# Kernel tuning notes

Hardware: AMD Instinct MI355X
Metric: run time of the kernel (lower is better)

## Reference

```python
import jax, jax.numpy as jnp
import numpy as np

N_A, N_C, N_L = 50000, 10000, 10000
HID = 128


def _gatv2(x_src, x_dst, src, dst, ea, Wl, bl, Wr, br, We, att, bias, H):
    # GATv2Conv (PyG) bipartite, edge_dim=1, concat=False (mean over heads), eval mode (no dropout)
    C = bias.shape[0]
    n_dst = x_dst.shape[0]
    xl = (x_src @ Wl + bl).reshape(-1, H, C)      # [N_src, H, C]
    xr = (x_dst @ Wr + br).reshape(-1, H, C)      # [N_dst, H, C]
    e = jax.nn.leaky_relu(xl[src] + xr[dst] + (ea @ We).reshape(-1, H, C), 0.2)  # [E,H,C]
    logit = jnp.einsum('ehc,hc->eh', e, att)      # [E,H]
    m = jax.ops.segment_max(logit, dst, num_segments=n_dst)
    m = jax.lax.stop_gradient(jnp.where(jnp.isfinite(m), m, 0.0))
    ex = jnp.exp(logit - m[dst])
    denom = jax.ops.segment_sum(ex, dst, num_segments=n_dst)
    alpha = ex / (denom[dst] + 1e-16)             # segment softmax over incoming edges
    out = jax.ops.segment_sum(alpha[:, :, None] * xl[src], dst, num_segments=n_dst)
    return out.mean(axis=1) + bias                # concat=False -> head mean + bias


def setup_inputs() -> dict:
    key = jax.random.key(0)
    ks = iter(jax.random.split(key, 80))
    def rn(shape, s=1.0):
        return jax.random.normal(next(ks), shape, jnp.float32) * s
    inp = {}
    inp['x_asset'] = rn((N_A, 512))
    inp['x_creator'] = rn((N_C, 2))
    inp['x_licensee'] = rn((N_L, 1))
    # edges: (name, E, src_max, dst_max)
    edges = [('cb', 50000, N_A, N_C), ('lt', 100000, N_A, N_L), ('sim', 200000, N_A, N_A),
             ('fw', 100000, N_A, N_A), ('rcb', 50000, N_C, N_A), ('rlt', 100000, N_L, N_A)]
    for name, E, smax, dmax in edges:
        inp[f'{name}_src'] = jax.random.randint(next(ks), (E,), 0, smax, jnp.int32)
        inp[f'{name}_dst'] = jax.random.randint(next(ks), (E,), 0, dmax, jnp.int32)
        inp[f'ea_{name}'] = rn((E, 1))
    w = 0.05  # param scale
    inp['Wp_a'] = rn((512, HID), w); inp['bp_a'] = rn((HID,), w)
    inp['Wp_c'] = rn((2, HID), w);   inp['bp_c'] = rn((HID,), w)
    inp['Wp_l'] = rn((1, HID), w);   inp['bp_l'] = rn((HID,), w)
    # layer 1: heads=2, stacked over the 6 relations
    H1 = 2
    inp['Wl1'] = rn((6, HID, H1 * HID), w); inp['bl1'] = rn((6, H1 * HID), w)
    inp['Wr1'] = rn((6, HID, H1 * HID), w); inp['br1'] = rn((6, H1 * HID), w)
    inp['We1'] = rn((6, 1, H1 * HID), w)
    inp['att1'] = rn((6, H1, HID), w); inp['bias1'] = rn((6, HID), w)
    # layer 2: heads=1
    inp['Wl2'] = rn((6, HID, HID), w); inp['bl2'] = rn((6, HID), w)
    inp['Wr2'] = rn((6, HID, HID), w); inp['br2'] = rn((6, HID), w)
    inp['We2'] = rn((6, 1, HID), w)
    inp['att2'] = rn((6, 1, HID), w); inp['bias2'] = rn((6, HID), w)
    inp['Wc1'] = rn((HID, HID), w); inp['bc1'] = rn((HID,), w)
    inp['Wc2'] = rn((HID, 3), w);   inp['bc2'] = rn((3,), w)
    inp['query_asset_index'] = 123
    return inp


def reference(x_asset, x_creator, x_licensee, Wp_a, bp_a, Wp_c, bp_c, Wp_l, bp_l,
              Wl1, bl1, Wr1, br1, We1, att1, bias1,
              Wl2, bl2, Wr2, br2, We2, att2, bias2,
              Wc1, bc1, Wc2, bc2,
              ea_cb, ea_lt, ea_sim, ea_fw, ea_rcb, ea_rlt,
              cb_src, cb_dst, lt_src, lt_dst, sim_src, sim_dst,
              fw_src, fw_dst, rcb_src, rcb_dst, rlt_src, rlt_dst,
              query_asset_index):
    x = {'Asset': x_asset @ Wp_a + bp_a,
         'Creator': x_creator @ Wp_c + bp_c,
         'Licensee': x_licensee @ Wp_l + bp_l}
    rels = [('Asset', 'Creator', cb_src, cb_dst, ea_cb),
            ('Asset', 'Licensee', lt_src, lt_dst, ea_lt),
            ('Asset', 'Asset', sim_src, sim_dst, ea_sim),
            ('Asset', 'Asset', fw_src, fw_dst, ea_fw),
            ('Creator', 'Asset', rcb_src, rcb_dst, ea_rcb),
            ('Licensee', 'Asset', rlt_src, rlt_dst, ea_rlt)]

    def hetero_layer(x, Wl, bl, Wr, br, We, att, bias, H):
        out = {k: jnp.zeros((v.shape[0], HID), v.dtype) for k, v in x.items()}
        for i, (st, dt, s, d, ea) in enumerate(rels):  # HeteroConv aggr='sum'
            out[dt] = out[dt] + _gatv2(x[st], x[dt], s, d, ea,
                                       Wl[i], bl[i], Wr[i], br[i], We[i], att[i], bias[i], H)
        return out

    x = hetero_layer(x, Wl1, bl1, Wr1, br1, We1, att1, bias1, 2)
    x = {k: jax.nn.relu(v) for k, v in x.items()}  # eval: dropout is identity
    x = hetero_layer(x, Wl2, bl2, Wr2, br2, We2, att2, bias2, 1)
    x = {k: jax.nn.relu(v) for k, v in x.items()}
    a = x['Asset'][query_asset_index]
    return jax.nn.relu(a @ Wc1 + bc1) @ Wc2 + bc2
```

## Files before the change

kernel.cpp:

```cpp
#include <hip/hip_runtime.h>
#include <math.h>

#define FAMAX 512
#define FCMAX 256
#define FLMAX 256
#define N1MAX 4096
#define N2MAX 512

struct Inputs {
  const float *x_asset, *x_creator, *x_licensee;
  const float *Wp_a,*bp_a,*Wp_c,*bp_c,*Wp_l,*bp_l;
  const float *Wl1,*bl1,*Wr1,*br1,*We1,*att1,*bias1;
  const float *Wl2,*bl2,*Wr2,*br2,*We2,*att2,*bias2;
  const float *Wc1,*bc1,*Wc2,*bc2;
};

struct Edges {
  const int *cb_s,*cb_d;  const float* ea_cb;  int Ecb;
  const int *lt_s,*lt_d;  const float* ea_lt;  int Elt;
  const int *sim_s,*sim_d;const float* ea_sim; int Esim;
  const int *fw_s,*fw_d;  const float* ea_fw;  int Efw;
  const int *rcb_s,*rcb_d;const float* ea_rcb; int Ercb;
  const int *rlt_s,*rlt_d;const float* ea_rlt; int Erlt;
};

struct WSP {
  int* cnt;
  int* flagA; int* flagC; int* flagL;
  int* fa; int* fc; int* fl;
  int* l2rel; int* l2src; float* l2ea;
  int* l1rel; int* l1src; int* l1dslot; float* l1ea;
  float* xr1a;
  float* xr1c;
  float* xr1l;
  float* xl1e;
  float* logit1;
  float* x1a;
  float* x1c;
  float* x1l;
  float* xr2q;
  float* xl2e;
  float* logit2;
};

__device__ __forceinline__ float leaky(float x){ return x > 0.f ? x : 0.2f*x; }

__device__ void proj_node(int type, int node, const Inputs& in, float* h0){
  int t = threadIdx.x;
  if (t < 128) {
    float acc;
    if (type == 0) {
      acc = in.bp_a[t];
      const float* xr = in.x_asset + (long long)node*512;
      for (int k=0;k<512;k++) acc = fmaf(xr[k], in.Wp_a[k*128+t], acc);
    } else if (type == 1) {
      acc = in.bp_c[t] + in.x_creator[node*2]*in.Wp_c[t] + in.x_creator[node*2+1]*in.Wp_c[128+t];
    } else {
      acc = in.bp_l[t] + in.x_licensee[node]*in.Wp_l[t];
    }
    h0[t] = acc;
  }
  __syncthreads();
}

__global__ void k1_scan_l2(Edges eg, const int* qptr, WSP w){
  int q = qptr[0];
  if (blockIdx.x==0 && threadIdx.x==0) w.flagA[q] = 1;
  int total = eg.Esim + eg.Efw + eg.Ercb + eg.Erlt;
  for (int i = blockIdx.x*blockDim.x + threadIdx.x; i < total; i += gridDim.x*blockDim.x){
    int j = i, rel; const int *sp,*dp; const float* ep;
    if (j < eg.Esim){ rel=2; sp=eg.sim_s; dp=eg.sim_d; ep=eg.ea_sim; }
    else { j -= eg.Esim;
      if (j < eg.Efw){ rel=3; sp=eg.fw_s; dp=eg.fw_d; ep=eg.ea_fw; }
      else { j -= eg.Efw;
        if (j < eg.Ercb){ rel=4; sp=eg.rcb_s; dp=eg.rcb_d; ep=eg.ea_rcb; }
        else { j -= eg.Ercb; rel=5; sp=eg.rlt_s; dp=eg.rlt_d; ep=eg.ea_rlt; }
      }
    }
    if (dp[j] == q){
      int src = sp[j];
      int k = atomicAdd(&w.cnt[0], 1);
      if (k < N2MAX){ w.l2rel[k]=rel; w.l2src[k]=src; w.l2ea[k]=ep[j]; }
      if (rel <= 3) w.flagA[src] = 1;
      else if (rel == 4) w.flagC[src] = 1;
      else w.flagL[src] = 1;
    }
  }
}

__global__ void k2_compact(WSP w){
  int i = blockIdx.x*blockDim.x + threadIdx.x;
  if (i < 50000){
    if (w.flagA[i] == 1){ int k = atomicAdd(&w.cnt[1],1);
      if (k < FAMAX){ w.flagA[i]=k+2; w.fa[k]=i; } else w.flagA[i]=0; }
  } else if (i < 60000){ int n=i-50000;
    if (w.flagC[n] == 1){ int k = atomicAdd(&w.cnt[2],1);
      if (k < FCMAX){ w.flagC[n]=k+2; w.fc[k]=n; } else w.flagC[n]=0; }
  } else if (i < 70000){ int n=i-60000;
    if (w.flagL[n] == 1){ int k = atomicAdd(&w.cnt[3],1);
      if (k < FLMAX){ w.flagL[n]=k+2; w.fl[k]=n; } else w.flagL[n]=0; }
  }
}

__global__ void k3_scan_l1(Edges eg, WSP w){
  int total = eg.Ecb+eg.Elt+eg.Esim+eg.Efw+eg.Ercb+eg.Erlt;
  for (int i = blockIdx.x*blockDim.x + threadIdx.x; i < total; i += gridDim.x*blockDim.x){
    int j = i, rel; const int *sp,*dp; const float* ep; const int* flag;
    if (j < eg.Ecb){ rel=0; sp=eg.cb_s; dp=eg.cb_d; ep=eg.ea_cb; flag=w.flagC; }
    else { j -= eg.Ecb;
    if (j < eg.Elt){ rel=1; sp=eg.lt_s; dp=eg.lt_d; ep=eg.ea_lt; flag=w.flagL; }
    else { j -= eg.Elt;
    if (j < eg.Esim){ rel=2; sp=eg.sim_s; dp=eg.sim_d; ep=eg.ea_sim; flag=w.flagA; }
    else { j -= eg.Esim;
    if (j < eg.Efw){ rel=3; sp=eg.fw_s; dp=eg.fw_d; ep=eg.ea_fw; flag=w.flagA; }
    else { j -= eg.Efw;
    if (j < eg.Ercb){ rel=4; sp=eg.rcb_s; dp=eg.rcb_d; ep=eg.ea_rcb; flag=w.flagA; }
    else { j -= eg.Ercb; rel=5; sp=eg.rlt_s; dp=eg.rlt_d; ep=eg.ea_rlt; flag=w.flagA; }}}}}
    int f = flag[dp[j]];
    if (f >= 2){
      int k = atomicAdd(&w.cnt[4], 1);
      if (k < N1MAX){ w.l1rel[k]=rel; w.l1src[k]=sp[j]; w.l1dslot[k]=f-2; w.l1ea[k]=ep[j]; }
    }
  }
}

__global__ void k4_xr1(Inputs in, WSP w){
  __shared__ float h0[128];
  int b = blockIdx.x;
  int na = w.cnt[1] < FAMAX ? w.cnt[1] : FAMAX;
  int nc = w.cnt[2] < FCMAX ? w.cnt[2] : FCMAX;
  int nl = w.cnt[3] < FLMAX ? w.cnt[3] : FLMAX;
  int rel; float* dst;
  if (b < FAMAX*4){
    int slot = b>>2, ridx = b&3;
    if (slot >= na) return;
    rel = 2 + ridx;
    proj_node(0, w.fa[slot], in, h0);
    dst = w.xr1a + ((size_t)slot*4 + ridx)*256;
  } else if (b < FAMAX*4 + FCMAX){
    int slot = b - FAMAX*4;
    if (slot >= nc) return;
    rel = 0;
    proj_node(1, w.fc[slot], in, h0);
    dst = w.xr1c + (size_t)slot*256;
  } else {
    int slot = b - FAMAX*4 - FCMAX;
    if (slot >= nl) return;
    rel = 1;
    proj_node(2, w.fl[slot], in, h0);
    dst = w.xr1l + (size_t)slot*256;
  }
  int j = threadIdx.x;
  float acc = in.br1[rel*256 + j];
  const float* W = in.Wr1 + (size_t)rel*128*256;
  for (int c=0;c<128;c++) acc = fmaf(h0[c], W[c*256 + j], acc);
  dst[j] = acc;
}

__global__ void k5_l1edge(Inputs in, WSP w){
  __shared__ float h0[128];
  __shared__ float red[256];
  int i = blockIdx.x;
  int n = w.cnt[4] < N1MAX ? w.cnt[4] : N1MAX;
  if (i >= n) return;
  int rel = w.l1rel[i], src = w.l1src[i], dslot = w.l1dslot[i];
  float ea = w.l1ea[i];
  int stype = (rel <= 3) ? 0 : (rel == 4 ? 1 : 2);
  proj_node(stype, src, in, h0);
  int j = threadIdx.x;
  float acc = in.bl1[rel*256 + j];
  const float* W = in.Wl1 + (size_t)rel*128*256;
  for (int c=0;c<128;c++) acc = fmaf(h0[c], W[c*256 + j], acc);
  w.xl1e[(size_t)i*256 + j] = acc;
  const float* xr;
  if (rel >= 2) xr = w.xr1a + ((size_t)dslot*4 + (rel-2))*256;
  else if (rel == 0) xr = w.xr1c + (size_t)dslot*256;
  else xr = w.xr1l + (size_t)dslot*256;
  float e = leaky(acc + xr[j] + ea*in.We1[rel*256 + j]);
  int h = j >> 7, c = j & 127;
  red[j] = e * in.att1[(rel*2 + h)*128 + c];
  __syncthreads();
  for (int s=64; s>0; s>>=1){ if (c < s) red[j] += red[j+s]; __syncthreads(); }
  if (c == 0) w.logit1[i*2 + h] = red[j];
}

__global__ void k6_agg(Inputs in, WSP w){
  int b = blockIdx.x;
  int na = w.cnt[1] < FAMAX ? w.cnt[1] : FAMAX;
  int nc = w.cnt[2] < FCMAX ? w.cnt[2] : FCMAX;
  int nl = w.cnt[3] < FLMAX ? w.cnt[3] : FLMAX;
  int type, slot;
  if (b < FAMAX){ slot = b; if (slot >= na) return; type = 0; }
  else if (b < FAMAX+FCMAX){ slot = b-FAMAX; if (slot >= nc) return; type = 1; }
  else { slot = b-FAMAX-FCMAX; if (slot >= nl) return; type = 2; }
  int n1 = w.cnt[4] < N1MAX ? w.cnt[4] : N1MAX;
  int j = threadIdx.x;
  float out = 0.f;
  int r0, r1;
  if (type == 0){ r0=2; r1=5; } else if (type == 1){ r0=0; r1=0; } else { r0=1; r1=1; }
  for (int r=r0; r<=r1; r++){
    out += in.bias1[r*128 + j];
    float m0 = -INFINITY, m1 = -INFINITY;
    for (int i=0;i<n1;i++){
      if (w.l1rel[i]==r && w.l1dslot[i]==slot){
        m0 = fmaxf(m0, w.logit1[i*2]);
        m1 = fmaxf(m1, w.logit1[i*2+1]);
      }
    }
    if (m0 == -INFINITY) continue;
    float d0=0.f, d1=0.f, a0=0.f, a1=0.f;
    for (int i=0;i<n1;i++){
      if (w.l1rel[i]==r && w.l1dslot[i]==slot){
        float e0 = expf(w.logit1[i*2]   - m0);
        float e1 = expf(w.logit1[i*2+1] - m1);
        d0 += e0; d1 += e1;
        a0 = fmaf(e0, w.xl1e[(size_t)i*256 + j], a0);
        a1 = fmaf(e1, w.xl1e[(size_t)i*256 + 128 + j], a1);
      }
    }
    out += 0.5f*(a0/(d0+1e-16f) + a1/(d1+1e-16f));
  }
  float v = fmaxf(out, 0.f);
  if (type == 0) w.x1a[slot*128 + j] = v;
  else if (type == 1) w.x1c[slot*128 + j] = v;
  else w.x1l[slot*128 + j] = v;
}

__global__ void k7_xr2(Inputs in, WSP w, const int* qptr){
  int q = qptr[0];
  int qslot = w.flagA[q] - 2;
  const float* xq = w.x1a + (size_t)qslot*128;
  int j = threadIdx.x;
  for (int ridx=0; ridx<4; ridx++){
    int r = 2 + ridx;
    float acc = in.br2[r*128 + j];
    const float* W = in.Wr2 + (size_t)r*128*128;
    for (int c=0;c<128;c++) acc = fmaf(xq[c], W[c*128 + j], acc);
    w.xr2q[ridx*128 + j] = acc;
  }
}

__global__ void k8_l2edge(Inputs in, WSP w){
  __shared__ float red[128];
  int i = blockIdx.x;
  int n2 = w.cnt[0] < N2MAX ? w.cnt[0] : N2MAX;
  if (i >= n2) return;
  int rel = w.l2rel[i], src = w.l2src[i];
  float ea = w.l2ea[i];
  int f;
  const float* xbase;
  if (rel <= 3){ f = w.flagA[src]; xbase = w.x1a; }
  else if (rel == 4){ f = w.flagC[src]; xbase = w.x1c; }
  else { f = w.flagL[src]; xbase = w.x1l; }
  if (f < 2) return;
  const float* xsrc = xbase + (size_t)(f-2)*128;
  int j = threadIdx.x;
  float acc = in.bl2[rel*128 + j];
  const float* W = in.Wl2 + (size_t)rel*128*128;
  for (int c=0;c<128;c++) acc = fmaf(xsrc[c], W[c*128 + j], acc);
  w.xl2e[(size_t)i*128 + j] = acc;
  float e = leaky(acc + w.xr2q[(rel-2)*128 + j] + ea*in.We2[rel*128 + j]);
  red[j] = e * in.att2[rel*128 + j];
  __syncthreads();
  for (int s=64; s>0; s>>=1){ if (j < s) red[j] += red[j+s]; __syncthreads(); }
  if (j == 0) w.logit2[i] = red[0];
}

__global__ void k9_final(Inputs in, WSP w, float* out){
  __shared__ float x2[128];
  __shared__ float t[128];
  int n2 = w.cnt[0] < N2MAX ? w.cnt[0] : N2MAX;
  int j = threadIdx.x;
  float o = 0.f;
  for (int r=2; r<=5; r++){
    o += in.bias2[r*128 + j];
    float m = -INFINITY;
    for (int i=0;i<n2;i++) if (w.l2rel[i]==r) m = fmaxf(m, w.logit2[i]);
    if (m == -INFINITY) continue;
    float d = 0.f, acc = 0.f;
    for (int i=0;i<n2;i++) if (w.l2rel[i]==r){
      float e = expf(w.logit2[i] - m);
      d += e;
      acc = fmaf(e, w.xl2e[(size_t)i*128 + j], acc);
    }
    o += acc/(d + 1e-16f);
  }
  x2[j] = fmaxf(o, 0.f);
  __syncthreads();
  float acc = in.bc1[j];
  for (int c=0;c<128;c++) acc = fmaf(x2[c], in.Wc1[c*128 + j], acc);
  t[j] = fmaxf(acc, 0.f);
  __syncthreads();
  if (j < 3){
    float r = in.bc2[j];
    for (int c=0;c<128;c++) r = fmaf(t[c], in.Wc2[c*3 + j], r);
    out[j] = r;
  }
}

extern "C" void kernel_launch(void* const* d_in, const int* in_sizes, int n_in,
                              void* d_out, int out_size, void* d_ws, size_t ws_size,
                              hipStream_t stream){
  Inputs in;
  in.x_asset   = (const float*)d_in[0];
  in.x_creator = (const float*)d_in[1];
  in.x_licensee= (const float*)d_in[2];
  Edges eg;
  eg.cb_s =(const int*)d_in[3];  eg.cb_d =(const int*)d_in[4];  eg.ea_cb =(const float*)d_in[5];  eg.Ecb = in_sizes[3];
  eg.lt_s =(const int*)d_in[6];  eg.lt_d =(const int*)d_in[7];  eg.ea_lt =(const float*)d_in[8];  eg.Elt = in_sizes[6];
  eg.sim_s=(const int*)d_in[9];  eg.sim_d=(const int*)d_in[10]; eg.ea_sim=(const float*)d_in[11]; eg.Esim= in_sizes[9];
  eg.fw_s =(const int*)d_in[12]; eg.fw_d =(const int*)d_in[13]; eg.ea_fw =(const float*)d_in[14]; eg.Efw = in_sizes[12];
  eg.rcb_s=(const int*)d_in[15]; eg.rcb_d=(const int*)d_in[16]; eg.ea_rcb=(const float*)d_in[17]; eg.Ercb= in_sizes[15];
  eg.rlt_s=(const int*)d_in[18]; eg.rlt_d=(const int*)d_in[19]; eg.ea_rlt=(const float*)d_in[20]; eg.Erlt= in_sizes[18];
  in.Wp_a=(const float*)d_in[21]; in.bp_a=(const float*)d_in[22];
  in.Wp_c=(const float*)d_in[23]; in.bp_c=(const float*)d_in[24];
  in.Wp_l=(const float*)d_in[25]; in.bp_l=(const float*)d_in[26];
  in.Wl1=(const float*)d_in[27]; in.bl1=(const float*)d_in[28];
  in.Wr1=(const float*)d_in[29]; in.br1=(const float*)d_in[30];
  in.We1=(const float*)d_in[31]; in.att1=(const float*)d_in[32]; in.bias1=(const float*)d_in[33];
  in.Wl2=(const float*)d_in[34]; in.bl2=(const float*)d_in[35];
  in.Wr2=(const float*)d_in[36]; in.br2=(const float*)d_in[37];
  in.We2=(const float*)d_in[38]; in.att2=(const float*)d_in[39]; in.bias2=(const float*)d_in[40];
  in.Wc1=(const float*)d_in[41]; in.bc1=(const float*)d_in[42];
  in.Wc2=(const float*)d_in[43]; in.bc2=(const float*)d_in[44];
  const int* qptr = (const int*)d_in[45];

  char* p = (char*)d_ws;
  auto carve = [&](size_t n)->char*{ char* r = p; p += ((n + 255) & ~(size_t)255); return r; };
  WSP w;
  w.cnt    = (int*)carve(16*4);
  w.flagA  = (int*)carve(50000*4);
  w.flagC  = (int*)carve(10000*4);
  w.flagL  = (int*)carve(10000*4);
  size_t zero_bytes = (size_t)(p - (char*)d_ws);
  w.fa = (int*)carve(FAMAX*4); w.fc = (int*)carve(FCMAX*4); w.fl = (int*)carve(FLMAX*4);
  w.l2rel=(int*)carve(N2MAX*4); w.l2src=(int*)carve(N2MAX*4); w.l2ea=(float*)carve(N2MAX*4);
  w.l1rel=(int*)carve(N1MAX*4); w.l1src=(int*)carve(N1MAX*4); w.l1dslot=(int*)carve(N1MAX*4); w.l1ea=(float*)carve(N1MAX*4);
  w.xr1a=(float*)carve((size_t)FAMAX*4*256*4);
  w.xr1c=(float*)carve((size_t)FCMAX*256*4);
  w.xr1l=(float*)carve((size_t)FLMAX*256*4);
  w.xl1e=(float*)carve((size_t)N1MAX*256*4);
  w.logit1=(float*)carve((size_t)N1MAX*2*4);
  w.x1a=(float*)carve((size_t)FAMAX*128*4);
  w.x1c=(float*)carve((size_t)FCMAX*128*4);
  w.x1l=(float*)carve((size_t)FLMAX*128*4);
  w.xr2q=(float*)carve(4*128*4);
  w.xl2e=(float*)carve((size_t)N2MAX*128*4);
  w.logit2=(float*)carve(N2MAX*4);

  hipMemsetAsync(d_ws, 0, zero_bytes, stream);

  int tE2 = eg.Esim + eg.Efw + eg.Ercb + eg.Erlt;
  k1_scan_l2<<<(tE2+255)/256, 256, 0, stream>>>(eg, qptr, w);
  k2_compact<<<(70000+255)/256, 256, 0, stream>>>(w);
  int tE1 = eg.Ecb + eg.Elt + tE2;
  k3_scan_l1<<<(tE1+255)/256, 256, 0, stream>>>(eg, w);
  k4_xr1<<<FAMAX*4 + FCMAX + FLMAX, 256, 0, stream>>>(in, w);
  k5_l1edge<<<N1MAX, 256, 0, stream>>>(in, w);
  k6_agg<<<FAMAX + FCMAX + FLMAX, 128, 0, stream>>>(in, w);
  k7_xr2<<<1, 128, 0, stream>>>(in, w, qptr);
  k8_l2edge<<<N2MAX, 128, 0, stream>>>(in, w);
  k9_final<<<1, 128, 0, stream>>>(in, w, (float*)d_out);
}
```

Before: 346.8 us.

## Deduplicate node projections into a shared table and shrink frontier capacities

```diff
diff --git a/kernel.cpp b/kernel.cpp
--- a/kernel.cpp
+++ b/kernel.cpp
@@ -1,11 +1,14 @@
 #include <hip/hip_runtime.h>
 #include <math.h>
 
-#define FAMAX 512
-#define FCMAX 256
-#define FLMAX 256
-#define N1MAX 4096
-#define N2MAX 512
+#define FAMAX 64
+#define FCMAX 32
+#define FLMAX 32
+#define PAMAX 256
+#define PCMAX 64
+#define PLMAX 64
+#define N1MAX 512
+#define N2MAX 128
 
 struct Inputs {
   const float *x_asset, *x_creator, *x_licensee;
@@ -26,18 +29,17 @@
 
 struct WSP {
   int* cnt;
-  int* flagA; int* flagC; int* flagL;
-  int* fa; int* fc; int* fl;
+  int *dfA,*dfC,*dfL;
+  int *pfA,*pfC,*pfL;
+  int *fa,*fc,*fl;
+  int *pa,*pc,*pl;
   int* l2rel; int* l2src; float* l2ea;
   int* l1rel; int* l1src; int* l1dslot; float* l1ea;
-  float* xr1a;
-  float* xr1c;
-  float* xr1l;
+  float *h0a,*h0c,*h0l;
+  float *xr1a,*xr1c,*xr1l;
   float* xl1e;
   float* logit1;
-  float* x1a;
-  float* x1c;
-  float* x1l;
+  float *x1a,*x1c,*x1l;
   float* xr2q;
   float* xl2e;
   float* logit2;
@@ -45,27 +47,21 @@
 
 __device__ __forceinline__ float leaky(float x){ return x > 0.f ? x : 0.2f*x; }
 
-__device__ void proj_node(int type, int node, const Inputs& in, float* h0){
-  int t = threadIdx.x;
-  if (t < 128) {
-    float acc;
-    if (type == 0) {
-      acc = in.bp_a[t];
-      const float* xr = in.x_asset + (long long)node*512;
-      for (int k=0;k<512;k++) acc = fmaf(xr[k], in.Wp_a[k*128+t], acc);
-    } else if (type == 1) {
-      acc = in.bp_c[t] + in.x_creator[node*2]*in.Wp_c[t] + in.x_creator[node*2+1]*in.Wp_c[128+t];
-    } else {
-      acc = in.bp_l[t] + in.x_licensee[node]*in.Wp_l[t];
-    }
-    h0[t] = acc;
-  }
-  __syncthreads();
+__device__ __forceinline__ void claim(int* flag, int* cnt, int* list, int node, int cap){
+  int old = atomicCAS(&flag[node], 0, 1);
+  if (old == 0){
+    int k = atomicAdd(cnt, 1);
+    if (k < cap){ list[k] = node; atomicExch(&flag[node], k + 2); }
+    else atomicExch(&flag[node], 0);
+  }
 }
 
 __global__ void k1_scan_l2(Edges eg, const int* qptr, WSP w){
   int q = qptr[0];
-  if (blockIdx.x==0 && threadIdx.x==0) w.flagA[q] = 1;
+  if (blockIdx.x==0 && threadIdx.x==0){
+    claim(w.dfA, &w.cnt[1], w.fa, q, FAMAX);
+    claim(w.pfA, &w.cnt[5], w.pa, q, PAMAX);
+  }
   int total = eg.Esim + eg.Efw + eg.Ercb + eg.Erlt;
   for (int i = blockIdx.x*blockDim.x + threadIdx.x; i < total; i += gridDim.x*blockDim.x){
     int j = i, rel; const int *sp,*dp; const float* ep;
@@ -81,126 +77,164 @@
       int src = sp[j];
       int k = atomicAdd(&w.cnt[0], 1);
       if (k < N2MAX){ w.l2rel[k]=rel; w.l2src[k]=src; w.l2ea[k]=ep[j]; }
-      if (rel <= 3) w.flagA[src] = 1;
-      else if (rel == 4) w.flagC[src] = 1;
-      else w.flagL[src] = 1;
-    }
-  }
-}
-
-__global__ void k2_compact(WSP w){
-  int i = blockIdx.x*blockDim.x + threadIdx.x;
-  if (i < 50000){
-    if (w.flagA[i] == 1){ int k = atomicAdd(&w.cnt[1],1);
-      if (k < FAMAX){ w.flagA[i]=k+2; w.fa[k]=i; } else w.flagA[i]=0; }
-  } else if (i < 60000){ int n=i-50000;
-    if (w.flagC[n] == 1){ int k = atomicAdd(&w.cnt[2],1);
-      if (k < FCMAX){ w.flagC[n]=k+2; w.fc[k]=n; } else w.flagC[n]=0; }
-  } else if (i < 70000){ int n=i-60000;
-    if (w.flagL[n] == 1){ int k = atomicAdd(&w.cnt[3],1);
-      if (k < FLMAX){ w.flagL[n]=k+2; w.fl[k]=n; } else w.flagL[n]=0; }
-  }
-}
-
-__global__ void k3_scan_l1(Edges eg, WSP w){
+      if (rel <= 3){ claim(w.dfA,&w.cnt[1],w.fa,src,FAMAX); claim(w.pfA,&w.cnt[5],w.pa,src,PAMAX); }
+      else if (rel == 4){ claim(w.dfC,&w.cnt[2],w.fc,src,FCMAX); claim(w.pfC,&w.cnt[6],w.pc,src,PCMAX); }
+      else { claim(w.dfL,&w.cnt[3],w.fl,src,FLMAX); claim(w.pfL,&w.cnt[7],w.pl,src,PLMAX); }
+    }
+  }
+}
+
+__global__ void k2_scan_l1(Edges eg, WSP w){
   int total = eg.Ecb+eg.Elt+eg.Esim+eg.Efw+eg.Ercb+eg.Erlt;
   for (int i = blockIdx.x*blockDim.x + threadIdx.x; i < total; i += gridDim.x*blockDim.x){
     int j = i, rel; const int *sp,*dp; const float* ep; const int* flag;
-    if (j < eg.Ecb){ rel=0; sp=eg.cb_s; dp=eg.cb_d; ep=eg.ea_cb; flag=w.flagC; }
+    if (j < eg.Ecb){ rel=0; sp=eg.cb_s; dp=eg.cb_d; ep=eg.ea_cb; flag=w.dfC; }
     else { j -= eg.Ecb;
-    if (j < eg.Elt){ rel=1; sp=eg.lt_s; dp=eg.lt_d; ep=eg.ea_lt; flag=w.flagL; }
+    if (j < eg.Elt){ rel=1; sp=eg.lt_s; dp=eg.lt_d; ep=eg.ea_lt; flag=w.dfL; }
     else { j -= eg.Elt;
-    if (j < eg.Esim){ rel=2; sp=eg.sim_s; dp=eg.sim_d; ep=eg.ea_sim; flag=w.flagA; }
+    if (j < eg.Esim){ rel=2; sp=eg.sim_s; dp=eg.sim_d; ep=eg.ea_sim; flag=w.dfA; }
     else { j -= eg.Esim;
-    if (j < eg.Efw){ rel=3; sp=eg.fw_s; dp=eg.fw_d; ep=eg.ea_fw; flag=w.flagA; }
+    if (j < eg.Efw){ rel=3; sp=eg.fw_s; dp=eg.fw_d; ep=eg.ea_fw; flag=w.dfA; }
     else { j -= eg.Efw;
-    if (j < eg.Ercb){ rel=4; sp=eg.rcb_s; dp=eg.rcb_d; ep=eg.ea_rcb; flag=w.flagA; }
-    else { j -= eg.Ercb; rel=5; sp=eg.rlt_s; dp=eg.rlt_d; ep=eg.ea_rlt; flag=w.flagA; }}}}}
+    if (j < eg.Ercb){ rel=4; sp=eg.rcb_s; dp=eg.rcb_d; ep=eg.ea_rcb; flag=w.dfA; }
+    else { j -= eg.Ercb; rel=5; sp=eg.rlt_s; dp=eg.rlt_d; ep=eg.ea_rlt; flag=w.dfA; }}}}}
     int f = flag[dp[j]];
     if (f >= 2){
+      int src = sp[j];
       int k = atomicAdd(&w.cnt[4], 1);
-      if (k < N1MAX){ w.l1rel[k]=rel; w.l1src[k]=sp[j]; w.l1dslot[k]=f-2; w.l1ea[k]=ep[j]; }
-    }
-  }
-}
-
-__global__ void k4_xr1(Inputs in, WSP w){
+      if (k < N1MAX){ w.l1rel[k]=rel; w.l1src[k]=src; w.l1dslot[k]=f-2; w.l1ea[k]=ep[j]; }
+      if (rel <= 3) claim(w.pfA,&w.cnt[5],w.pa,src,PAMAX);
+      else if (rel == 4) claim(w.pfC,&w.cnt[6],w.pc,src,PCMAX);
+      else claim(w.pfL,&w.cnt[7],w.pl,src,PLMAX);
+    }
+  }
+}
+
+__global__ void k3a_proj(Inputs in, WSP w){
+  int b = blockIdx.x, t = threadIdx.x;
+  if (b < PAMAX){
+    __shared__ float xs[512];
+    __shared__ float part[512];
+    int npa = w.cnt[5] < PAMAX ? w.cnt[5] : PAMAX;
+    if (b >= npa) return;
+    int node = w.pa[b];
+    xs[t] = in.x_asset[(size_t)node*512 + t];
+    __syncthreads();
+    int j = t & 127, g = t >> 7;
+    float acc = 0.f;
+    const float* W = in.Wp_a + (size_t)g*128*128 + j;
+    const float* xg = xs + g*128;
+    for (int k=0;k<128;k++) acc = fmaf(xg[k], W[(size_t)k*128], acc);
+    part[t] = acc;
+    __syncthreads();
+    if (t < 128)
+      w.h0a[(size_t)b*128 + t] = in.bp_a[t] + part[t] + part[128+t] + part[256+t] + part[384+t];
+  } else if (b == PAMAX){
+    int npc = w.cnt[6] < PCMAX ? w.cnt[6] : PCMAX;
+    int j = t & 127, s0 = t >> 7;
+    for (int s = s0; s < npc; s += 4){
+      int node = w.pc[s];
+      w.h0c[s*128 + j] = in.bp_c[j] + in.x_creator[node*2]*in.Wp_c[j]
+                       + in.x_creator[node*2+1]*in.Wp_c[128+j];
+    }
+  } else {
+    int npl = w.cnt[7] < PLMAX ? w.cnt[7] : PLMAX;
+    int j = t & 127, s0 = t >> 7;
+    for (int s = s0; s < npl; s += 4){
+      int node = w.pl[s];
+      w.h0l[s*128 + j] = in.bp_l[j] + in.x_licensee[node]*in.Wp_l[j];
+    }
+  }
+}
+
+__global__ void k3b_xr1(Inputs in, WSP w){
   __shared__ float h0[128];
-  int b = blockIdx.x;
-  int na = w.cnt[1] < FAMAX ? w.cnt[1] : FAMAX;
-  int nc = w.cnt[2] < FCMAX ? w.cnt[2] : FCMAX;
-  int nl = w.cnt[3] < FLMAX ? w.cnt[3] : FLMAX;
-  int rel; float* dst;
+  int b = blockIdx.x, t = threadIdx.x;
+  int rel; const float* hsrc; float* dst;
   if (b < FAMAX*4){
-    int slot = b>>2, ridx = b&3;
-    if (slot >= na) return;
+    int slot = b >> 2, ridx = b & 3;
+    int nfa = w.cnt[1] < FAMAX ? w.cnt[1] : FAMAX;
+    if (slot >= nfa) return;
     rel = 2 + ridx;
-    proj_node(0, w.fa[slot], in, h0);
+    int ps = w.pfA[w.fa[slot]] - 2; if (ps < 0) return;
+    hsrc = w.h0a + (size_t)ps*128;
     dst = w.xr1a + ((size_t)slot*4 + ridx)*256;
   } else if (b < FAMAX*4 + FCMAX){
     int slot = b - FAMAX*4;
-    if (slot >= nc) return;
+    int nfc = w.cnt[2] < FCMAX ? w.cnt[2] : FCMAX;
+    if (slot >= nfc) return;
     rel = 0;
-    proj_node(1, w.fc[slot], in, h0);
+    int ps = w.pfC[w.fc[slot]] - 2; if (ps < 0) return;
+    hsrc = w.h0c + (size_t)ps*128;
     dst = w.xr1c + (size_t)slot*256;
   } else {
     int slot = b - FAMAX*4 - FCMAX;
-    if (slot >= nl) return;
+    int nfl = w.cnt[3] < FLMAX ? w.cnt[3] : FLMAX;
+    if (slot >= nfl) return;
     rel = 1;
-    proj_node(2, w.fl[slot], in, h0);
+    int ps = w.pfL[w.fl[slot]] - 2; if (ps < 0) return;
+    hsrc = w.h0l + (size_t)ps*128;
     dst = w.xr1l + (size_t)slot*256;
   }
-  int j = threadIdx.x;
-  float acc = in.br1[rel*256 + j];
-  const float* W = in.Wr1 + (size_t)rel*128*256;
-  for (int c=0;c<128;c++) acc = fmaf(h0[c], W[c*256 + j], acc);
-  dst[j] = acc;
-}
-
-__global__ void k5_l1edge(Inputs in, WSP w){
+  if (t < 128) h0[t] = hsrc[t];
+  __syncthreads();
+  float acc = in.br1[rel*256 + t];
+  const float* W = in.Wr1 + (size_t)rel*128*256 + t;
+  for (int c=0;c<128;c++) acc = fmaf(h0[c], W[(size_t)c*256], acc);
+  dst[t] = acc;
+}
+
+__global__ void k3c_edge(Inputs in, WSP w){
   __shared__ float h0[128];
   __shared__ float red[256];
-  int i = blockIdx.x;
-  int n = w.cnt[4] < N1MAX ? w.cnt[4] : N1MAX;
-  if (i >= n) return;
+  int i = blockIdx.x, t = threadIdx.x;
+  int n1 = w.cnt[4] < N1MAX ? w.cnt[4] : N1MAX;
+  if (i >= n1) return;
   int rel = w.l1rel[i], src = w.l1src[i], dslot = w.l1dslot[i];
   float ea = w.l1ea[i];
-  int stype = (rel <= 3) ? 0 : (rel == 4 ? 1 : 2);
-  proj_node(stype, src, in, h0);
-  int j = threadIdx.x;
-  float acc = in.bl1[rel*256 + j];
-  const float* W = in.Wl1 + (size_t)rel*128*256;
-  for (int c=0;c<128;c++) acc = fmaf(h0[c], W[c*256 + j], acc);
-  w.xl1e[(size_t)i*256 + j] = acc;
+  int ps; const float* hsrc;
+  if (rel <= 3){ ps = w.pfA[src]-2; hsrc = w.h0a + (size_t)(ps>0?ps:0)*128; }
+  else if (rel == 4){ ps = w.pfC[src]-2; hsrc = w.h0c + (size_t)(ps>0?ps:0)*128; }
+  else { ps = w.pfL[src]-2; hsrc = w.h0l + (size_t)(ps>0?ps:0)*128; }
+  if (ps < 0){
+    w.xl1e[(size_t)i*256 + t] = 0.f;
+    if (t < 2) w.logit1[i*2 + t] = -INFINITY;
+    return;
+  }
+  if (t < 128) h0[t] = hsrc[t];
+  __syncthreads();
+  float acc = in.bl1[rel*256 + t];
+  const float* W = in.Wl1 + (size_t)rel*128*256 + t;
+  for (int c=0;c<128;c++) acc = fmaf(h0[c], W[(size_t)c*256], acc);
+  w.xl1e[(size_t)i*256 + t] = acc;
   const float* xr;
   if (rel >= 2) xr = w.xr1a + ((size_t)dslot*4 + (rel-2))*256;
   else if (rel == 0) xr = w.xr1c + (size_t)dslot*256;
   else xr = w.xr1l + (size_t)dslot*256;
-  float e = leaky(acc + xr[j] + ea*in.We1[rel*256 + j]);
-  int h = j >> 7, c = j & 127;
-  red[j] = e * in.att1[(rel*2 + h)*128 + c];
-  __syncthreads();
-  for (int s=64; s>0; s>>=1){ if (c < s) red[j] += red[j+s]; __syncthreads(); }
-  if (c == 0) w.logit1[i*2 + h] = red[j];
-}
-
-__global__ void k6_agg(Inputs in, WSP w){
-  int b = blockIdx.x;
-  int na = w.cnt[1] < FAMAX ? w.cnt[1] : FAMAX;
-  int nc = w.cnt[2] < FCMAX ? w.cnt[2] : FCMAX;
-  int nl = w.cnt[3] < FLMAX ? w.cnt[3] : FLMAX;
+  int h = t >> 7, c = t & 127;
+  float e = leaky(acc + xr[t] + ea*in.We1[rel*256 + t]);
+  red[t] = e * in.att1[(rel*2 + h)*128 + c];
+  __syncthreads();
+  for (int s=64; s>0; s>>=1){ if (c < s) red[t] += red[t+s]; __syncthreads(); }
+  if (c == 0) w.logit1[i*2 + h] = red[t];
+}
+
+__global__ void k4_agg(Inputs in, WSP w){
+  int b = blockIdx.x, j = threadIdx.x;
+  int nfa = w.cnt[1] < FAMAX ? w.cnt[1] : FAMAX;
+  int nfc = w.cnt[2] < FCMAX ? w.cnt[2] : FCMAX;
+  int nfl = w.cnt[3] < FLMAX ? w.cnt[3] : FLMAX;
   int type, slot;
-  if (b < FAMAX){ slot = b; if (slot >= na) return; type = 0; }
-  else if (b < FAMAX+FCMAX){ slot = b-FAMAX; if (slot >= nc) return; type = 1; }
-  else { slot = b-FAMAX-FCMAX; if (slot >= nl) return; type = 2; }
+  if (b < FAMAX){ slot=b; if (slot>=nfa) return; type=0; }
+  else if (b < FAMAX+FCMAX){ slot=b-FAMAX; if (slot>=nfc) return; type=1; }
+  else { slot=b-FAMAX-FCMAX; if (slot>=nfl) return; type=2; }
   int n1 = w.cnt[4] < N1MAX ? w.cnt[4] : N1MAX;
-  int j = threadIdx.x;
   float out = 0.f;
   int r0, r1;
-  if (type == 0){ r0=2; r1=5; } else if (type == 1){ r0=0; r1=0; } else { r0=1; r1=1; }
+  if (type==0){ r0=2; r1=5; } else if (type==1){ r0=0; r1=0; } else { r0=1; r1=1; }
   for (int r=r0; r<=r1; r++){
     out += in.bias1[r*128 + j];
-    float m0 = -INFINITY, m1 = -INFINITY;
+    float m0=-INFINITY, m1=-INFINITY;
     for (int i=0;i<n1;i++){
       if (w.l1rel[i]==r && w.l1dslot[i]==slot){
         m0 = fmaxf(m0, w.logit1[i*2]);
@@ -214,50 +248,55 @@
         float e0 = expf(w.logit1[i*2]   - m0);
         float e1 = expf(w.logit1[i*2+1] - m1);
         d0 += e0; d1 += e1;
-        a0 = fmaf(e0, w.xl1e[(size_t)i*256 + j], a0);
+        a0 = fmaf(e0, w.xl1e[(size_t)i*256 + j],       a0);
         a1 = fmaf(e1, w.xl1e[(size_t)i*256 + 128 + j], a1);
       }
     }
     out += 0.5f*(a0/(d0+1e-16f) + a1/(d1+1e-16f));
   }
   float v = fmaxf(out, 0.f);
-  if (type == 0) w.x1a[slot*128 + j] = v;
-  else if (type == 1) w.x1c[slot*128 + j] = v;
+  if (type==0) w.x1a[slot*128 + j] = v;
+  else if (type==1) w.x1c[slot*128 + j] = v;
   else w.x1l[slot*128 + j] = v;
 }
 
-__global__ void k7_xr2(Inputs in, WSP w, const int* qptr){
+__global__ void k5a_xr2(Inputs in, WSP w, const int* qptr){
+  __shared__ float xq[128];
+  int t = threadIdx.x;
   int q = qptr[0];
-  int qslot = w.flagA[q] - 2;
-  const float* xq = w.x1a + (size_t)qslot*128;
-  int j = threadIdx.x;
-  for (int ridx=0; ridx<4; ridx++){
-    int r = 2 + ridx;
-    float acc = in.br2[r*128 + j];
-    const float* W = in.Wr2 + (size_t)r*128*128;
-    for (int c=0;c<128;c++) acc = fmaf(xq[c], W[c*128 + j], acc);
-    w.xr2q[ridx*128 + j] = acc;
-  }
-}
-
-__global__ void k8_l2edge(Inputs in, WSP w){
+  int qs = w.dfA[q] - 2;
+  if (t < 128) xq[t] = w.x1a[(size_t)qs*128 + t];
+  __syncthreads();
+  int ridx = t >> 7, j = t & 127;
+  int r = 2 + ridx;
+  float acc = in.br2[r*128 + j];
+  const float* W = in.Wr2 + (size_t)r*128*128 + j;
+  for (int c=0;c<128;c++) acc = fmaf(xq[c], W[(size_t)c*128], acc);
+  w.xr2q[ridx*128 + j] = acc;
+}
+
+__global__ void k5b_l2edge(Inputs in, WSP w){
+  __shared__ float xs[128];
   __shared__ float red[128];
-  int i = blockIdx.x;
+  int i = blockIdx.x, j = threadIdx.x;
   int n2 = w.cnt[0] < N2MAX ? w.cnt[0] : N2MAX;
   if (i >= n2) return;
   int rel = w.l2rel[i], src = w.l2src[i];
   float ea = w.l2ea[i];
-  int f;
-  const float* xbase;
-  if (rel <= 3){ f = w.flagA[src]; xbase = w.x1a; }
-  else if (rel == 4){ f = w.flagC[src]; xbase = w.x1c; }
-  else { f = w.flagL[src]; xbase = w.x1l; }
-  if (f < 2) return;
-  const float* xsrc = xbase + (size_t)(f-2)*128;
-  int j = threadIdx.x;
+  int f; const float* xb;
+  if (rel <= 3){ f = w.dfA[src]; xb = w.x1a; }
+  else if (rel == 4){ f = w.dfC[src]; xb = w.x1c; }
+  else { f = w.dfL[src]; xb = w.x1l; }
+  if (f < 2){
+    w.xl2e[(size_t)i*128 + j] = 0.f;
+    if (j == 0) w.logit2[i] = -INFINITY;
+    return;
+  }
+  xs[j] = xb[(size_t)(f-2)*128 + j];
+  __syncthreads();
   float acc = in.bl2[rel*128 + j];
-  const float* W = in.Wl2 + (size_t)rel*128*128;
-  for (int c=0;c<128;c++) acc = fmaf(xsrc[c], W[c*128 + j], acc);
+  const float* W = in.Wl2 + (size_t)rel*128*128 + j;
+  for (int c=0;c<128;c++) acc = fmaf(xs[c], W[(size_t)c*128], acc);
   w.xl2e[(size_t)i*128 + j] = acc;
   float e = leaky(acc + w.xr2q[(rel-2)*128 + j] + ea*in.We2[rel*128 + j]);
   red[j] = e * in.att2[rel*128 + j];
@@ -266,11 +305,11 @@
   if (j == 0) w.logit2[i] = red[0];
 }
 
-__global__ void k9_final(Inputs in, WSP w, float* out){
+__global__ void k5c_final(Inputs in, WSP w, float* outp){
   __shared__ float x2[128];
-  __shared__ float t[128];
+  __shared__ float tt[128];
+  int j = threadIdx.x;
   int n2 = w.cnt[0] < N2MAX ? w.cnt[0] : N2MAX;
-  int j = threadIdx.x;
   float o = 0.f;
   for (int r=2; r<=5; r++){
     o += in.bias2[r*128 + j];
@@ -289,12 +328,12 @@
   __syncthreads();
   float acc = in.bc1[j];
   for (int c=0;c<128;c++) acc = fmaf(x2[c], in.Wc1[c*128 + j], acc);
-  t[j] = fmaxf(acc, 0.f);
+  tt[j] = fmaxf(acc, 0.f);
   __syncthreads();
   if (j < 3){
     float r = in.bc2[j];
-    for (int c=0;c<128;c++) r = fmaf(t[c], in.Wc2[c*3 + j], r);
-    out[j] = r;
+    for (int c=0;c<128;c++) r = fmaf(tt[c], in.Wc2[c*3 + j], r);
+    outp[j] = r;
   }
 }
 
@@ -328,14 +367,17 @@
   char* p = (char*)d_ws;
   auto carve = [&](size_t n)->char*{ char* r = p; p += ((n + 255) & ~(size_t)255); return r; };
   WSP w;
-  w.cnt    = (int*)carve(16*4);
-  w.flagA  = (int*)carve(50000*4);
-  w.flagC  = (int*)carve(10000*4);
-  w.flagL  = (int*)carve(10000*4);
+  w.cnt  = (int*)carve(16*4);
+  w.dfA  = (int*)carve(50000*4); w.dfC = (int*)carve(10000*4); w.dfL = (int*)carve(10000*4);
+  w.pfA  = (int*)carve(50000*4); w.pfC = (int*)carve(10000*4); w.pfL = (int*)carve(10000*4);
   size_t zero_bytes = (size_t)(p - (char*)d_ws);
   w.fa = (int*)carve(FAMAX*4); w.fc = (int*)carve(FCMAX*4); w.fl = (int*)carve(FLMAX*4);
+  w.pa = (int*)carve(PAMAX*4); w.pc = (int*)carve(PCMAX*4); w.pl = (int*)carve(PLMAX*4);
   w.l2rel=(int*)carve(N2MAX*4); w.l2src=(int*)carve(N2MAX*4); w.l2ea=(float*)carve(N2MAX*4);
   w.l1rel=(int*)carve(N1MAX*4); w.l1src=(int*)carve(N1MAX*4); w.l1dslot=(int*)carve(N1MAX*4); w.l1ea=(float*)carve(N1MAX*4);
+  w.h0a=(float*)carve((size_t)PAMAX*128*4);
+  w.h0c=(float*)carve((size_t)PCMAX*128*4);
+  w.h0l=(float*)carve((size_t)PLMAX*128*4);
   w.xr1a=(float*)carve((size_t)FAMAX*4*256*4);
   w.xr1c=(float*)carve((size_t)FCMAX*256*4);
   w.xr1l=(float*)carve((size_t)FLMAX*256*4);
@@ -352,13 +394,13 @@
 
   int tE2 = eg.Esim + eg.Efw + eg.Ercb + eg.Erlt;
   k1_scan_l2<<<(tE2+255)/256, 256, 0, stream>>>(eg, qptr, w);
-  k2_compact<<<(70000+255)/256, 256, 0, stream>>>(w);
   int tE1 = eg.Ecb + eg.Elt + tE2;
-  k3_scan_l1<<<(tE1+255)/256, 256, 0, stream>>>(eg, w);
-  k4_xr1<<<FAMAX*4 + FCMAX + FLMAX, 256, 0, stream>>>(in, w);
-  k5_l1edge<<<N1MAX, 256, 0, stream>>>(in, w);
-  k6_agg<<<FAMAX + FCMAX + FLMAX, 128, 0, stream>>>(in, w);
-  k7_xr2<<<1, 128, 0, stream>>>(in, w, qptr);
-  k8_l2edge<<<N2MAX, 128, 0, stream>>>(in, w);
-  k9_final<<<1, 128, 0, stream>>>(in, w, (float*)d_out);
-}
+  k2_scan_l1<<<(tE1+255)/256, 256, 0, stream>>>(eg, w);
+  k3a_proj<<<PAMAX+2, 512, 0, stream>>>(in, w);
+  k3b_xr1<<<FAMAX*4 + FCMAX + FLMAX, 256, 0, stream>>>(in, w);
+  k3c_edge<<<N1MAX, 256, 0, stream>>>(in, w);
+  k4_agg<<<FAMAX + FCMAX + FLMAX, 128, 0, stream>>>(in, w);
+  k5a_xr2<<<1, 512, 0, stream>>>(in, w, qptr);
+  k5b_l2edge<<<N2MAX, 128, 0, stream>>>(in, w);
+  k5c_final<<<1, 128, 0, stream>>>(in, w, (float*)d_out);
+}
```

After: 309.6 us. 10.7% less time.
